# Performance work log

Hardware: AMD Instinct MI355X
Metric: run time of the kernel (lower is better)

Reference implementation:

```python
import jax, jax.numpy as jnp
import numpy as np

DIM = 192
NUM_HEADS = 4
B, H, W = 2, 256, 256
EPS = 1e-12  # torch F.normalize default eps


def setup_inputs() -> dict:
    key = jax.random.key(0)
    k1, k2, k3 = jax.random.split(key, 3)
    x = jax.random.normal(k1, (B, DIM, H, W), dtype=jnp.float32)
    # depthwise qkv conv: groups=DIM, each group maps 1 in-ch -> 3 out-ch; torch OIHW layout (3*DIM, 1, 3, 3)
    w_qkv = jax.random.normal(k2, (3 * DIM, 1, 3, 3), dtype=jnp.float32) * 0.1
    temperature = jnp.ones((NUM_HEADS, 1, 1), dtype=jnp.float32)
    # 1x1 projection conv, stored as [out, in]
    w_proj = jax.random.normal(k3, (DIM, DIM), dtype=jnp.float32) * (1.0 / np.sqrt(DIM))
    return {"x": x, "w_qkv": w_qkv, "temperature": temperature, "w_proj": w_proj}


def reference(x, w_qkv, temperature, w_proj):
    b, c, h, w = x.shape
    num_heads = temperature.shape[0]
    ch = c // num_heads  # channels per head
    # grouped (depthwise) 3x3 conv producing qkv; torch grouped-conv channel order
    # matches feature_group_count ordering (3 consecutive out-chs per group)... but
    # note torch chunk(3, dim=1) splits the 3*c output into contiguous thirds, so
    # q gets out-channels [0, c), etc. We replicate exactly with same layout.
    qkv = jax.lax.conv_general_dilated(
        x, w_qkv, window_strides=(1, 1), padding=((1, 1), (1, 1)),
        feature_group_count=c,
        dimension_numbers=("NCHW", "OIHW", "NCHW"))
    q, k, v = jnp.split(qkv, 3, axis=1)  # each [b, c, h, w]
    q = q.reshape(b, num_heads, ch, h * w)
    k = k.reshape(b, num_heads, ch, h * w)
    v = v.reshape(b, num_heads, ch, h * w)
    # L2 normalize along spatial dim (torch F.normalize with eps clamp)
    q = q / jnp.maximum(jnp.linalg.norm(q, axis=-1, keepdims=True), EPS)
    k = k / jnp.maximum(jnp.linalg.norm(k, axis=-1, keepdims=True), EPS)
    # channel-channel cosine attention, [b, head, ch, ch] (small)
    attn = jnp.einsum("bhcn,bhdn->bhcd", q, k) * temperature
    attn = jax.nn.softmax(attn, axis=-1)
    out = jnp.einsum("bhcd,bhdn->bhcn", attn, v).reshape(b, c, h, w)
    # 1x1 projection conv
    out = jnp.einsum("oi,bihw->bohw", w_proj, out)
    return out
```

## Files before the change

kernel.cpp:

```cpp
#include <hip/hip_runtime.h>
#include <math.h>

#define BB 2
#define CC 192
#define NH 4
#define CH 48
#define SRCP 16
#define HH 256
#define WW 256
#define NPIX (HH*WW)

typedef __attribute__((ext_vector_type(8))) short short8;
typedef __attribute__((ext_vector_type(4))) float f4;

static __device__ __forceinline__ unsigned short f2bf(float f) {
    union { float f; unsigned int u; } c; c.f = f;
    unsigned int r = c.u + 0x7fffu + ((c.u >> 16) & 1u);
    return (unsigned short)(r >> 16);
}

__global__ __launch_bounds__(256, 3) void k_conv(
    const float* __restrict__ x, const float* __restrict__ wqkv,
    unsigned short* __restrict__ vws, float* __restrict__ Sws,
    float* __restrict__ sqws)
{
    __shared__ unsigned int qk32[2][CH][132];

    const int tid = threadIdx.x;
    const int hd = blockIdx.x;
    const int y  = blockIdx.y;
    const int b  = blockIdx.z;

    {
        const int xp = tid;
        const int y0 = (y > 0) ? (y-1) : 0;
        const int y2 = (y < HH-1) ? (y+1) : y;
        const int xl = (xp > 0) ? (xp-1) : 0;
        const int xr = (xp < WW-1) ? (xp+1) : xp;
        const float my0 = (y > 0) ? 1.f : 0.f;
        const float my2 = (y < HH-1) ? 1.f : 0.f;
        const float mx0 = (xp > 0) ? 1.f : 0.f;
        const float mx2 = (xp < WW-1) ? 1.f : 0.f;
        const float m00 = my0*mx0, m02 = my0*mx2, m20 = my2*mx0, m22 = my2*mx2;

        #pragma unroll
        for (int type = 0; type < 2; ++type) {
            const int srcbase = type*64 + SRCP*hd;
            const float* wt = wqkv + type*(CC*9) + hd*(CH*9);
            for (int g4 = 0; g4 < SRCP; g4 += 4) {
                float A[4][9];
                #pragma unroll
                for (int u = 0; u < 4; ++u) {
                    const float* base = x + ((size_t)(b*CC + srcbase + g4 + u)*HH)*WW;
                    const float* r0 = base + (size_t)y0*WW;
                    const float* r1 = base + (size_t)y *WW;
                    const float* r2 = base + (size_t)y2*WW;
                    A[u][0] = r0[xl]; A[u][1] = r0[xp]; A[u][2] = r0[xr];
                    A[u][3] = r1[xl]; A[u][4] = r1[xp]; A[u][5] = r1[xr];
                    A[u][6] = r2[xl]; A[u][7] = r2[xp]; A[u][8] = r2[xr];
                }
                #pragma unroll
                for (int u = 0; u < 4; ++u) {
                    const int g = g4 + u;
                    float a00 = A[u][0]*m00, a01 = A[u][1]*my0, a02 = A[u][2]*m02;
                    float a10 = A[u][3]*mx0, a11 = A[u][4],     a12 = A[u][5]*mx2;
                    float a20 = A[u][6]*m20, a21 = A[u][7]*my2, a22 = A[u][8]*m22;
                    #pragma unroll
                    for (int r = 0; r < 3; ++r) {
                        const int cl = 3*g + r;
                        const float* w = wt + cl*9;
                        float val = a00*w[0] + a01*w[1] + a02*w[2]
                                  + a10*w[3] + a11*w[4] + a12*w[5]
                                  + a20*w[6] + a21*w[7] + a22*w[8];
                        ((unsigned short*)&qk32[type][cl][0])[xp] = f2bf(val);
                    }
                }
            }
        }

        unsigned int vpack[24];
        {
            const int srcbase = 128 + SRCP*hd;
            const float* wt = wqkv + 2*(CC*9) + hd*(CH*9);
            #pragma unroll
            for (int g4 = 0; g4 < SRCP; g4 += 4) {
                float A[4][9];
                #pragma unroll
                for (int u = 0; u < 4; ++u) {
                    const float* base = x + ((size_t)(b*CC + srcbase + g4 + u)*HH)*WW;
                    const float* r0 = base + (size_t)y0*WW;
                    const float* r1 = base + (size_t)y *WW;
                    const float* r2 = base + (size_t)y2*WW;
                    A[u][0] = r0[xl]; A[u][1] = r0[xp]; A[u][2] = r0[xr];
                    A[u][3] = r1[xl]; A[u][4] = r1[xp]; A[u][5] = r1[xr];
                    A[u][6] = r2[xl]; A[u][7] = r2[xp]; A[u][8] = r2[xr];
                }
                #pragma unroll
                for (int u = 0; u < 4; ++u) {
                    const int g = g4 + u;
                    float a00 = A[u][0]*m00, a01 = A[u][1]*my0, a02 = A[u][2]*m02;
                    float a10 = A[u][3]*mx0, a11 = A[u][4],     a12 = A[u][5]*mx2;
                    float a20 = A[u][6]*m20, a21 = A[u][7]*my2, a22 = A[u][8]*m22;
                    #pragma unroll
                    for (int r = 0; r < 3; ++r) {
                        const int cl = 3*g + r;
                        const float* w = wt + cl*9;
                        float val = a00*w[0] + a01*w[1] + a02*w[2]
                                  + a10*w[3] + a11*w[4] + a12*w[5]
                                  + a20*w[6] + a21*w[7] + a22*w[8];
                        unsigned int uu = f2bf(val);
                        if (cl & 1) vpack[cl >> 1] |= (uu << 16);
                        else        vpack[cl >> 1]  = uu;
                    }
                }
            }
        }
        {
            unsigned short* vp = vws + ((size_t)b*NPIX + (size_t)y*WW + xp)*CC + hd*CH;
            #pragma unroll
            for (int st = 0; st < 6; ++st) {
                uint4 u; u.x = vpack[st*4+0]; u.y = vpack[st*4+1];
                         u.z = vpack[st*4+2]; u.w = vpack[st*4+3];
                *(uint4*)(vp + st*8) = u;
            }
        }
    }
    __syncthreads();

    if (tid < 2*CH) {
        const int which = tid / CH;
        const int cl = tid - which*CH;
        const uint4* row = (const uint4*)&qk32[which][cl][0];
        float ssum = 0.f;
        for (int j = 0; j < 32; ++j) {
            uint4 u = row[j];
            #pragma unroll
            for (int q4 = 0; q4 < 4; ++q4) {
                unsigned int w = (&u.x)[q4];
                float lo = __uint_as_float(w << 16);
                float hi = __uint_as_float(w & 0xffff0000u);
                ssum = fmaf(lo, lo, ssum);
                ssum = fmaf(hi, hi, ssum);
            }
        }
        atomicAdd(&sqws[((b*NH + hd)*2 + which)*CH + cl], ssum);
    }

    {
        const int lane = tid & 63;
        const int wv = tid >> 6;
        const int m = lane & 15, quad = lane >> 4;
        for (int p = wv; p < 9; p += 4) {
            const int ct = p / 3, dt = p - ct*3;
            f4 acc = {0.f, 0.f, 0.f, 0.f};
            const char* qbase = (const char*)&qk32[0][ct*16 + m][0] + quad*16;
            const char* kbase = (const char*)&qk32[1][dt*16 + m][0] + quad*16;
            #pragma unroll
            for (int ks = 0; ks < 8; ++ks) {
                short8 afr = *(const short8*)(qbase + ks*64);
                short8 bfr = *(const short8*)(kbase + ks*64);
                acc = __builtin_amdgcn_mfma_f32_16x16x32_bf16(afr, bfr, acc, 0, 0, 0);
            }
            const int c0 = ct*16 + quad*4, d = dt*16 + m;
            float* Sp = Sws + ((size_t)(b*NH + hd)*CH + c0)*CH + d;
            #pragma unroll
            for (int r = 0; r < 4; ++r) atomicAdd(Sp + r*CH, acc[r]);
        }
    }
}

__global__ __launch_bounds__(256) void k_attn(
    const float* __restrict__ Sws, const float* __restrict__ sqws,
    const float* __restrict__ temp, const float* __restrict__ wproj,
    unsigned short* __restrict__ W2bf)
{
    __shared__ float att[CH][CH+1];
    __shared__ float wp[CC][CH+1];
    __shared__ float nrm[2][CH];

    const int tid = threadIdx.x;
    const int b  = blockIdx.x >> 2;
    const int hd = blockIdx.x & 3;

    if (tid < 2*CH) {
        int which = tid / CH, cl = tid - which*CH;
        nrm[which][cl] = fmaxf(sqrtf(sqws[((b*NH + hd)*2 + which)*CH + cl]), 1e-12f);
    }
    __syncthreads();

    const float tscale = temp[hd];
    for (int m = tid; m < CH*CH; m += 256) {
        int c = m / CH, d = m - c*CH;
        att[c][d] = Sws[((size_t)(b*NH + hd)*CH + c)*CH + d] * tscale
                    / (nrm[0][c] * nrm[1][d]);
    }
    __syncthreads();

    if (tid < CH) {
        float mx = -1e30f;
        for (int d = 0; d < CH; ++d) mx = fmaxf(mx, att[tid][d]);
        float sm = 0.f;
        for (int d = 0; d < CH; ++d) { float e = expf(att[tid][d] - mx); att[tid][d] = e; sm += e; }
        float inv = 1.f / sm;
        for (int d = 0; d < CH; ++d) att[tid][d] *= inv;
    }

    for (int m = tid; m < CC*CH; m += 256) {
        int o = m / CH, il = m - o*CH;
        wp[o][il] = wproj[o*CC + hd*CH + il];
    }
    __syncthreads();

    const int o0  = (tid & 31) * 6;
    const int dl0 = (tid >> 5) * 6;
    float a[6][6];
    #pragma unroll
    for (int i = 0; i < 6; ++i)
        #pragma unroll
        for (int j = 0; j < 6; ++j) a[i][j] = 0.f;
    for (int il = 0; il < CH; ++il) {
        float wv[6], av[6];
        #pragma unroll
        for (int i = 0; i < 6; ++i) wv[i] = wp[o0+i][il];
        #pragma unroll
        for (int j = 0; j < 6; ++j) av[j] = att[il][dl0+j];
        #pragma unroll
        for (int i = 0; i < 6; ++i)
            #pragma unroll
            for (int j = 0; j < 6; ++j)
                a[i][j] = fmaf(wv[i], av[j], a[i][j]);
    }
    #pragma unroll
    for (int i = 0; i < 6; ++i)
        #pragma unroll
        for (int j = 0; j < 6; ++j)
            W2bf[((size_t)b*CC + o0 + i)*CC + hd*CH + dl0 + j] = f2bf(a[i][j]);
}

__global__ __launch_bounds__(256, 3) void k_out(
    const unsigned short* __restrict__ vws, const unsigned short* __restrict__ W2bf,
    float* __restrict__ out)
{
    const int tid = threadIdx.x;
    const int b  = blockIdx.y;
    const int n0 = blockIdx.x * 128;

    const int lane = tid & 63;
    const int wv = tid >> 6;
    const int m0  = (wv & 1) * 96;
    const int nn0 = (wv >> 1) * 64;
    const int m = lane & 15, quad = lane >> 4;

    f4 acc[6][4];
    #pragma unroll
    for (int mt = 0; mt < 6; ++mt)
        #pragma unroll
        for (int nt = 0; nt < 4; ++nt) acc[mt][nt] = (f4){0.f, 0.f, 0.f, 0.f};

    const unsigned short* vb = vws + ((size_t)b*NPIX + n0 + nn0 + m)*CC + quad*8;
    const unsigned short* wb = W2bf + ((size_t)(b*CC + m0 + m))*CC + quad*8;

    #pragma unroll
    for (int ks = 0; ks < 6; ++ks) {
        short8 bfr[4];
        #pragma unroll
        for (int nt = 0; nt < 4; ++nt)
            bfr[nt] = *(const short8*)(vb + (size_t)(nt*16)*CC + ks*32);
        short8 afr[6];
        #pragma unroll
        for (int mt = 0; mt < 6; ++mt)
            afr[mt] = *(const short8*)(wb + (size_t)(mt*16)*CC + ks*32);
        #pragma unroll
        for (int mt = 0; mt < 6; ++mt)
            #pragma unroll
            for (int nt = 0; nt < 4; ++nt)
                acc[mt][nt] = __builtin_amdgcn_mfma_f32_16x16x32_bf16(afr[mt], bfr[nt], acc[mt][nt], 0, 0, 0);
    }

    #pragma unroll
    for (int mt = 0; mt < 6; ++mt) {
        const int o = m0 + mt*16 + quad*4;
        #pragma unroll
        for (int nt = 0; nt < 4; ++nt) {
            const int px = n0 + nn0 + nt*16 + m;
            float* op = out + ((size_t)(b*CC + o))*NPIX + px;
            #pragma unroll
            for (int r = 0; r < 4; ++r) op[(size_t)r*NPIX] = acc[mt][nt][r];
        }
    }
}

extern "C" void kernel_launch(void* const* d_in, const int* in_sizes, int n_in,
                              void* d_out, int out_size, void* d_ws, size_t ws_size,
                              hipStream_t stream)
{
    const float* x     = (const float*)d_in[0];
    const float* wqkv  = (const float*)d_in[1];
    const float* temp  = (const float*)d_in[2];
    const float* wproj = (const float*)d_in[3];
    float* out = (float*)d_out;
    (void)in_sizes; (void)n_in; (void)out_size; (void)ws_size;

    unsigned short* vws = (unsigned short*)d_ws;
    const size_t VBYTES = (size_t)BB*CC*NPIX*sizeof(unsigned short);
    float* Sws  = (float*)((char*)d_ws + VBYTES);
    float* sqws = Sws + (size_t)BB*NH*CH*CH;
    unsigned short* W2bf = (unsigned short*)(sqws + (size_t)BB*NH*2*CH);

    hipMemsetAsync(Sws, 0, (size_t)(BB*NH*CH*CH + BB*NH*2*CH)*sizeof(float), stream);
    k_conv<<<dim3(NH, HH, BB), 256, 0, stream>>>(x, wqkv, vws, Sws, sqws);
    k_attn<<<dim3(BB*NH), 256, 0, stream>>>(Sws, sqws, temp, wproj, W2bf);
    k_out<<<dim3(NPIX/128, BB), 256, 0, stream>>>(vws, W2bf, out);
}
```

Before: 309.5 us.

## Stage W2 in LDS and transpose output through LDS for vector stores

```diff
diff --git a/kernel.cpp b/kernel.cpp
--- a/kernel.cpp
+++ b/kernel.cpp
@@ -237,13 +237,24 @@
             W2bf[((size_t)b*CC + o0 + i)*CC + hd*CH + dl0 + j] = f2bf(a[i][j]);
 }
 
-__global__ __launch_bounds__(256, 3) void k_out(
+__global__ __launch_bounds__(256, 2) void k_out(
     const unsigned short* __restrict__ vws, const unsigned short* __restrict__ W2bf,
     float* __restrict__ out)
 {
+    __shared__ unsigned short w2l[CC][200];
+
     const int tid = threadIdx.x;
     const int b  = blockIdx.y;
     const int n0 = blockIdx.x * 128;
+
+    {
+        const uint4* src = (const uint4*)(W2bf + (size_t)b*CC*CC);
+        for (int i = tid; i < CC*24; i += 256) {
+            int o = i / 24, c = i - o*24;
+            *(uint4*)&w2l[o][c*8] = src[i];
+        }
+    }
+    __syncthreads();
 
     const int lane = tid & 63;
     const int wv = tid >> 6;
@@ -258,7 +269,6 @@
         for (int nt = 0; nt < 4; ++nt) acc[mt][nt] = (f4){0.f, 0.f, 0.f, 0.f};
 
     const unsigned short* vb = vws + ((size_t)b*NPIX + n0 + nn0 + m)*CC + quad*8;
-    const unsigned short* wb = W2bf + ((size_t)(b*CC + m0 + m))*CC + quad*8;
 
     #pragma unroll
     for (int ks = 0; ks < 6; ++ks) {
@@ -269,7 +279,7 @@
         short8 afr[6];
         #pragma unroll
         for (int mt = 0; mt < 6; ++mt)
-            afr[mt] = *(const short8*)(wb + (size_t)(mt*16)*CC + ks*32);
+            afr[mt] = *(const short8*)&w2l[m0 + mt*16 + m][ks*32 + quad*8];
         #pragma unroll
         for (int mt = 0; mt < 6; ++mt)
             #pragma unroll
@@ -277,15 +287,35 @@
                 acc[mt][nt] = __builtin_amdgcn_mfma_f32_16x16x32_bf16(afr[mt], bfr[nt], acc[mt][nt], 0, 0, 0);
     }
 
-    #pragma unroll
-    for (int mt = 0; mt < 6; ++mt) {
-        const int o = m0 + mt*16 + quad*4;
-        #pragma unroll
-        for (int nt = 0; nt < 4; ++nt) {
-            const int px = n0 + nn0 + nt*16 + m;
-            float* op = out + ((size_t)(b*CC + o))*NPIX + px;
-            #pragma unroll
-            for (int r = 0; r < 4; ++r) op[(size_t)r*NPIX] = acc[mt][nt][r];
+    float* trsp = (float*)w2l;
+    const int orow = lane >> 2;
+    const int seg  = (lane & 3) * 16;
+
+    #pragma unroll
+    for (int ph = 0; ph < 2; ++ph) {
+        const int mtb = ph * 3;
+        __syncthreads();
+        #pragma unroll
+        for (int mtl = 0; mtl < 3; ++mtl)
+            #pragma unroll
+            for (int nt = 0; nt < 4; ++nt)
+                #pragma unroll
+                for (int r = 0; r < 4; ++r)
+                    trsp[((wv*3 + mtl)*16 + quad*4 + r)*68 + nt*16 + m] = acc[mtb+mtl][nt][r];
+        __syncthreads();
+        #pragma unroll
+        for (int mtl = 0; mtl < 3; ++mtl) {
+            const float* srcp = &trsp[((wv*3 + mtl)*16 + orow)*68 + seg];
+            f4 d0 = *(const f4*)(srcp + 0);
+            f4 d1 = *(const f4*)(srcp + 4);
+            f4 d2 = *(const f4*)(srcp + 8);
+            f4 d3 = *(const f4*)(srcp + 12);
+            const int o = m0 + (mtb + mtl)*16 + orow;
+            float* op = out + ((size_t)(b*CC + o))*NPIX + n0 + nn0 + seg;
+            *(f4*)(op + 0)  = d0;
+            *(f4*)(op + 4)  = d1;
+            *(f4*)(op + 8)  = d2;
+            *(f4*)(op + 12) = d3;
         }
     }
 }
```

Result: no change. 313.6 us (+1.3%).
